# Performance work log

Hardware: AMD Instinct MI355X
Metric: run time of the kernel (lower is better)

## Reference

```python
import jax, jax.numpy as jnp
import numpy as np

EPS = 1e-5
GROUPS = 32


def group_norm(x, gamma, beta):
    b, c, h, w = x.shape
    xg = x.reshape(b, GROUPS, c // GROUPS, h, w)
    mu = xg.mean(axis=(2, 3, 4), keepdims=True)
    var = xg.var(axis=(2, 3, 4), keepdims=True)
    xn = ((xg - mu) * jax.lax.rsqrt(var + EPS)).reshape(b, c, h, w)
    return xn * gamma[None, :, None, None] + beta[None, :, None, None]


def setup_inputs() -> dict:
    key = jax.random.key(0)
    ks = jax.random.split(key, 4)
    b, c, h, w = 4, 512, 64, 64
    x = jax.random.normal(ks[0], (b, c, h, w), dtype=jnp.float32)
    gn_w = jnp.ones((c,), jnp.float32)
    gn_b = jnp.zeros((c,), jnp.float32)
    qkv_w = jax.random.normal(ks[1], (3 * c, c), dtype=jnp.float32) * (c ** -0.5)
    qkv_b = jnp.zeros((3 * c,), jnp.float32)
    out_w = jax.random.normal(ks[2], (c, c), dtype=jnp.float32) * (c ** -0.5)
    out_b = jnp.zeros((c,), jnp.float32)
    return {"x": x, "gn_w": gn_w, "gn_b": gn_b, "qkv_w": qkv_w,
            "qkv_b": qkv_b, "out_w": out_w, "out_b": out_b}


def reference(x, gn_w, gn_b, qkv_w, qkv_b, out_w, out_b):
    b, c, hh, ww = x.shape
    n = hh * ww
    h = group_norm(x, gn_w, gn_b)
    # 1x1 conv == per-pixel matmul over channels
    qkv = jnp.einsum('bchw,oc->bohw', h, qkv_w) + qkv_b[None, :, None, None]
    q, k, v = jnp.split(qkv, 3, axis=1)
    q = q.transpose(0, 2, 3, 1).reshape(b, n, c)   # (b, n, c)
    k = k.reshape(b, c, n)                          # (b, c, n)
    v = v.transpose(0, 2, 3, 1).reshape(b, n, c)   # (b, n, c)
    attn = jax.nn.softmax(jnp.einsum('bnc,bcm->bnm', q, k) * (c ** -0.5), axis=-1)
    out = jnp.einsum('bnm,bmc->bnc', attn, v)
    out = out.reshape(b, hh, ww, c).transpose(0, 3, 1, 2)
    out = jnp.einsum('bchw,oc->bohw', out, out_w) + out_b[None, :, None, None]
    return out + x
```

## Files before the change

kernel.cpp:

```cpp
#include <hip/hip_runtime.h>
#include <cmath>

#define NB 4
#define NC 512
#define NN 4096
#define ATTN_SCALE 0.04419417382415922f

typedef __bf16 bf16x8 __attribute__((ext_vector_type(8)));
typedef float floatx4 __attribute__((ext_vector_type(4)));

__device__ __forceinline__ unsigned short f2bf(float f) {
    union { float f; unsigned int u; } v; v.f = f;
    return (unsigned short)((v.u + 0x7fffu + ((v.u >> 16) & 1u)) >> 16);
}
__device__ __forceinline__ unsigned short f2bf_trunc(float f) {
    union { float f; unsigned int u; } v; v.f = f;
    return (unsigned short)(v.u >> 16);
}
__device__ __forceinline__ float bf2f(unsigned short u) {
    union { unsigned int u; float f; } v; v.u = ((unsigned int)u) << 16;
    return v.f;
}

__device__ __forceinline__ void gload_lds16(const unsigned short* gp, unsigned short* lp) {
    __builtin_amdgcn_global_load_lds(
        (const __attribute__((address_space(1))) void*)gp,
        (__attribute__((address_space(3))) void*)lp, 16, 0, 0);
}

__global__ __launch_bounds__(256) void gn_partial_kernel(
    const float* __restrict__ x, float* __restrict__ part)
{
    int blk = blockIdx.x;
    int bg = blk >> 3, sub = blk & 7;
    const float4* xv = (const float4*)(x + (size_t)bg * 16 * NN + (size_t)sub * 8192);
    float s1 = 0.f, s2 = 0.f;
#pragma unroll
    for (int i = 0; i < 8; ++i) {
        float4 v = xv[threadIdx.x + i * 256];
        s1 += v.x + v.y + v.z + v.w;
        s2 += v.x * v.x + v.y * v.y + v.z * v.z + v.w * v.w;
    }
#pragma unroll
    for (int off = 32; off; off >>= 1) {
        s1 += __shfl_xor(s1, off, 64);
        s2 += __shfl_xor(s2, off, 64);
    }
    __shared__ float r1[4], r2[4];
    int lane = threadIdx.x & 63, w = threadIdx.x >> 6;
    if (lane == 0) { r1[w] = s1; r2[w] = s2; }
    __syncthreads();
    if (threadIdx.x == 0) {
        part[blk * 2]     = r1[0] + r1[1] + r1[2] + r1[3];
        part[blk * 2 + 1] = r2[0] + r2[1] + r2[2] + r2[3];
    }
}

__global__ __launch_bounds__(128) void gn_final_kernel(
    const float* __restrict__ part, const float* __restrict__ gw,
    const float* __restrict__ gb, float* __restrict__ ss)
{
    int tg = threadIdx.x;
    int b = tg >> 5, g = tg & 31;
    float s1 = 0.f, s2 = 0.f;
#pragma unroll
    for (int s = 0; s < 8; ++s) {
        s1 += part[(tg * 8 + s) * 2];
        s2 += part[(tg * 8 + s) * 2 + 1];
    }
    float mean = s1 * (1.0f / 65536.0f);
    float var  = s2 * (1.0f / 65536.0f) - mean * mean;
    float rstd = rsqrtf(var + 1e-5f);
#pragma unroll
    for (int i = 0; i < 16; ++i) {
        int c = g * 16 + i;
        float sc = rstd * gw[c];
        ss[b * NC + c] = sc;
        ss[2048 + b * NC + c] = gb[c] - mean * sc;
    }
}

__global__ __launch_bounds__(256) void wconv_kernel(
    const float* __restrict__ qkv_w, const float* __restrict__ out_w,
    unsigned short* __restrict__ wq, unsigned short* __restrict__ wo)
{
    int i = blockIdx.x * 256 + threadIdx.x;
    const int NQ = 1536 * 512;
    if (i < NQ) wq[i] = f2bf(qkv_w[i]);
    else        wo[i - NQ] = f2bf(out_w[i - NQ]);
}

__global__ __launch_bounds__(256) void htnorm_kernel(
    const float* __restrict__ x, const float* __restrict__ ss,
    unsigned short* __restrict__ ht)
{
    int b = blockIdx.z;
    int c0 = blockIdx.y * 32, n0 = blockIdx.x * 32;
    __shared__ float T[32][33];
    int tx = threadIdx.x & 31, ty = threadIdx.x >> 5;
    const float* xb = x + ((size_t)b * NC + c0) * NN;
    const float* sc = ss + b * NC + c0;
    const float* sh = ss + 2048 + b * NC + c0;
#pragma unroll
    for (int i = 0; i < 4; ++i) {
        int c = ty + i * 8;
        T[c][tx] = xb[(size_t)c * NN + n0 + tx] * sc[c] + sh[c];
    }
    __syncthreads();
    unsigned short* hb = ht + ((size_t)b * NN + n0) * NC + c0;
#pragma unroll
    for (int i = 0; i < 4; ++i) {
        int n = ty + i * 8;
        hb[(size_t)n * NC + tx] = f2bf(T[tx][n]);
    }
}

template<int MODE, int BM, int BN>
__global__ __launch_bounds__(256, 3) void mfma_gemm(
    const unsigned short* __restrict__ Abase,
    const unsigned short* __restrict__ Bbase,
    const float* __restrict__ e0, const float* __restrict__ e1,
    float* __restrict__ outf,
    unsigned short* __restrict__ ob0, unsigned short* __restrict__ ob1)
{
    constexpr int K = 512;
    constexpr int FI = BM / 32;
    constexpr int FJ = BN / 32;
    const int z = blockIdx.z;
    const size_t bnc = (size_t)NN * NC;
    const size_t bss = (size_t)NN * NN;

    const unsigned short* A;
    const unsigned short* B;
    if constexpr (MODE == 0)      { A = Abase + (size_t)z * bnc; B = Bbase; }
    else if constexpr (MODE == 1) { A = Abase; B = Bbase + (size_t)z * bnc; }
    else if constexpr (MODE == 2) { A = Abase + (size_t)z * bnc; B = Bbase + (size_t)z * bnc; }
    else                          { A = Abase; B = Bbase + (size_t)z * bnc; }

    const int m0 = blockIdx.y * BM;
    const int n0 = blockIdx.x * BN;

    __shared__ __attribute__((aligned(16))) unsigned short As[BM * 32];
    __shared__ __attribute__((aligned(16))) unsigned short Bs[BN * 32];

    const int t = threadIdx.x;
    const int lane = t & 63;
    const int w = t >> 6;
    const int wr = w >> 1, wc = w & 1;

    const int sr = w * 16 + (lane >> 2);
    const int sc8 = (lane & 3) * 8;
    const int lds_elem = w * 512;

    floatx4 acc[FI][FJ] = {};

    for (int k0 = 0; k0 < K; k0 += 32) {
#pragma unroll
        for (int s = 0; s < BM / 64; ++s)
            gload_lds16(A + (size_t)(m0 + s * 64 + sr) * K + k0 + sc8,
                        As + s * 2048 + lds_elem);
#pragma unroll
        for (int s = 0; s < BN / 64; ++s)
            gload_lds16(B + (size_t)(n0 + s * 64 + sr) * K + k0 + sc8,
                        Bs + s * 2048 + lds_elem);
        __syncthreads();

        bf16x8 af[FI], bfr[FJ];
        const unsigned short* Ab = As + ((wr * (BM / 2) + (lane & 15)) * 32) + (lane >> 4) * 8;
        const unsigned short* Bb = Bs + ((wc * (BN / 2) + (lane & 15)) * 32) + (lane >> 4) * 8;
#pragma unroll
        for (int i = 0; i < FI; ++i) af[i]  = *(const bf16x8*)(Ab + i * 16 * 32);
#pragma unroll
        for (int j = 0; j < FJ; ++j) bfr[j] = *(const bf16x8*)(Bb + j * 16 * 32);
#pragma unroll
        for (int i = 0; i < FI; ++i)
#pragma unroll
            for (int j = 0; j < FJ; ++j)
                acc[i][j] = __builtin_amdgcn_mfma_f32_16x16x32_bf16(
                    af[i], bfr[j], acc[i][j], 0, 0, 0);
        __syncthreads();
    }

    const int fr = lane >> 4;
    const int fc = lane & 15;

    if constexpr (MODE == 2) {
        float rs[FI][4];
#pragma unroll
        for (int i = 0; i < FI; ++i)
#pragma unroll
            for (int r = 0; r < 4; ++r) rs[i][r] = 0.f;
#pragma unroll
        for (int i = 0; i < FI; ++i) {
#pragma unroll
            for (int j = 0; j < FJ; ++j) {
                int n = n0 + wc * (BN / 2) + j * 16 + fc;
                int mbase = m0 + wr * (BM / 2) + i * 16 + fr * 4;
#pragma unroll
                for (int r = 0; r < 4; ++r) {
                    float e = __expf(acc[i][j][r]);
                    ob0[(size_t)z * bss + (size_t)(mbase + r) * NN + n] = f2bf_trunc(e);
                    rs[i][r] += e;
                }
            }
        }
#pragma unroll
        for (int i = 0; i < FI; ++i) {
#pragma unroll
            for (int r = 0; r < 4; ++r) {
                float v = rs[i][r];
                v += __shfl_xor(v, 1, 16);
                v += __shfl_xor(v, 2, 16);
                v += __shfl_xor(v, 4, 16);
                v += __shfl_xor(v, 8, 16);
                if (fc == 0) {
                    int m = m0 + wr * (BM / 2) + i * 16 + fr * 4 + r;
                    atomicAdd(&outf[z * NN + m], v);
                }
            }
        }
        return;
    }

#pragma unroll
    for (int i = 0; i < FI; ++i) {
#pragma unroll
        for (int j = 0; j < FJ; ++j) {
            int n = n0 + wc * (BN / 2) + j * 16 + fc;
            int mbase = m0 + wr * (BM / 2) + i * 16 + fr * 4;
#pragma unroll
            for (int r = 0; r < 4; ++r) {
                int m = mbase + r;
                float val = acc[i][j][r];
                if constexpr (MODE == 0) {
                    val += e0[n];
                    if (n < 512) ob0[((size_t)z * NN + m) * NC + n] = f2bf(val * ATTN_SCALE);
                    else         ob1[((size_t)z * NN + m) * NC + (n - 512)] = f2bf(val);
                } else if constexpr (MODE == 1) {
                    val += e0[1024 + m];
                    ob0[((size_t)z * NC + m) * NN + n] = f2bf(val);
                } else {
                    size_t idx = ((size_t)z * NC + m) * NN + n;
                    outf[idx] = val + e0[m] + e1[idx];
                }
            }
        }
    }
}

__global__ __launch_bounds__(256, 3) void pv_gemm(
    const unsigned short* __restrict__ Abase,
    const unsigned short* __restrict__ Bbase,
    const float* __restrict__ L,
    unsigned short* __restrict__ Ob)
{
    const int z = blockIdx.z;
    const size_t bss = (size_t)NN * NN, bnc = (size_t)NN * NC;
    const unsigned short* A = Abase + (size_t)z * bss;
    const unsigned short* B = Bbase + (size_t)z * bnc;
    const int m0 = blockIdx.y * 64;
    const int n0 = blockIdx.x * 256;

    __shared__ __attribute__((aligned(16))) unsigned short As[64 * 32];
    __shared__ __attribute__((aligned(16))) unsigned short Bs[256 * 32];

    const int t = threadIdx.x;
    const int lane = t & 63;
    const int w = t >> 6;
    const int wr = w >> 1, wc = w & 1;
    const int sr = w * 16 + (lane >> 2);
    const int sc8 = (lane & 3) * 8;
    const int lds_elem = w * 512;

    floatx4 acc[2][8] = {};

    for (int k0 = 0; k0 < NN; k0 += 32) {
        gload_lds16(A + (size_t)(m0 + sr) * NN + k0 + sc8, As + lds_elem);
#pragma unroll
        for (int s = 0; s < 4; ++s)
            gload_lds16(B + (size_t)(n0 + s * 64 + sr) * NN + k0 + sc8,
                        Bs + s * 2048 + lds_elem);
        __syncthreads();

        bf16x8 af[2], bfr[8];
        const unsigned short* Ab = As + ((wr * 32 + (lane & 15)) * 32) + (lane >> 4) * 8;
        const unsigned short* Bb = Bs + ((wc * 128 + (lane & 15)) * 32) + (lane >> 4) * 8;
#pragma unroll
        for (int i = 0; i < 2; ++i) af[i]  = *(const bf16x8*)(Ab + i * 16 * 32);
#pragma unroll
        for (int j = 0; j < 8; ++j) bfr[j] = *(const bf16x8*)(Bb + j * 16 * 32);
#pragma unroll
        for (int i = 0; i < 2; ++i)
#pragma unroll
            for (int j = 0; j < 8; ++j)
                acc[i][j] = __builtin_amdgcn_mfma_f32_16x16x32_bf16(
                    af[i], bfr[j], acc[i][j], 0, 0, 0);
        __syncthreads();
    }

    const int fr = lane >> 4;
    const int fc = lane & 15;
#pragma unroll
    for (int i = 0; i < 2; ++i) {
#pragma unroll
        for (int r = 0; r < 4; ++r) {
            int m = m0 + wr * 32 + i * 16 + fr * 4 + r;
            float linv = 1.0f / L[z * NN + m];
#pragma unroll
            for (int j = 0; j < 8; ++j) {
                int n = n0 + wc * 128 + j * 16 + fc;
                Ob[(size_t)z * bnc + (size_t)m * NC + n] = f2bf(acc[i][j][r] * linv);
            }
        }
    }
}

extern "C" void kernel_launch(void* const* d_in, const int* in_sizes, int n_in,
                              void* d_out, int out_size, void* d_ws, size_t ws_size,
                              hipStream_t stream)
{
    const float* x     = (const float*)d_in[0];
    const float* gn_w  = (const float*)d_in[1];
    const float* gn_b  = (const float*)d_in[2];
    const float* qkv_w = (const float*)d_in[3];
    const float* qkv_b = (const float*)d_in[4];
    const float* out_w = (const float*)d_in[5];
    const float* out_b = (const float*)d_in[6];
    float* out = (float*)d_out;

    const size_t bnc = (size_t)NN * NC;
    char* w = (char*)d_ws;
    float* ss   = (float*)w;                 w += 16384;
    float* part = (float*)w;                 w += 8192;
    float* Lsum = (float*)w;                 w += (size_t)NB * NN * 4;
    unsigned short* wq = (unsigned short*)w; w += (size_t)1536 * 512 * 2;
    unsigned short* wo = (unsigned short*)w; w += (size_t)512 * 512 * 2;
    unsigned short* qt = (unsigned short*)w; w += NB * bnc * 2;
    unsigned short* kt = (unsigned short*)w; w += NB * bnc * 2;
    unsigned short* vt = (unsigned short*)w; w += NB * bnc * 2;
    unsigned short* SP = (unsigned short*)w; w += (size_t)NB * NN * NN * 2;
    unsigned short* ht = SP;
    unsigned short* Ob = qt;

    hipMemsetAsync(Lsum, 0, (size_t)NB * NN * sizeof(float), stream);

    gn_partial_kernel<<<1024, 256, 0, stream>>>(x, part);
    gn_final_kernel<<<1, 128, 0, stream>>>(part, gn_w, gn_b, ss);
    wconv_kernel<<<(1536 * 512 + 512 * 512) / 256, 256, 0, stream>>>(qkv_w, out_w, wq, wo);
    htnorm_kernel<<<dim3(NN / 32, NC / 32, NB), 256, 0, stream>>>(x, ss, ht);

    mfma_gemm<0, 128, 128><<<dim3(1024 / 128, NN / 128, NB), 256, 0, stream>>>(
        ht, wq, qkv_b, nullptr, nullptr, qt, kt);
    mfma_gemm<1, 128, 128><<<dim3(NN / 128, 512 / 128, NB), 256, 0, stream>>>(
        wq + (size_t)1024 * 512, ht, qkv_b, nullptr, nullptr, vt, nullptr);

    mfma_gemm<2, 128, 128><<<dim3(NN / 128, NN / 128, NB), 256, 0, stream>>>(
        qt, kt, nullptr, nullptr, Lsum, SP, nullptr);
    pv_gemm<<<dim3(512 / 256, NN / 64, NB), 256, 0, stream>>>(SP, vt, Lsum, Ob);

    mfma_gemm<4, 128, 128><<<dim3(NN / 128, 512 / 128, NB), 256, 0, stream>>>(
        wo, Ob, out_b, x, out, nullptr, nullptr);
}
```

Measured before the change: 412.0 us.

## Retile PV GEMM with XOR-swizzled LDS, deeper K step, and XCD-aware block mapping

The P·V GEMM moves from a 64x256 tile with K=32 to a 64x128 tile with K=64, using an XOR swizzle on the LDS row layout to avoid bank conflicts on fragment reads. The grid is flattened to 1024 blocks and remapped so the four column tiles sharing the same P rows land on the same XCD, improving L2 reuse of the large SP matrix. Occupancy target rises to 4 blocks/SM with fewer accumulators. Narrower tiles mean SP rows are read twice as often overall, relying on cache locality to offset that.

```diff
diff --git a/kernel.cpp b/kernel.cpp
--- a/kernel.cpp
+++ b/kernel.cpp
@@ -248,53 +248,76 @@
     }
 }
 
-__global__ __launch_bounds__(256, 3) void pv_gemm(
+__global__ __launch_bounds__(256, 4) void pv_gemm(
     const unsigned short* __restrict__ Abase,
     const unsigned short* __restrict__ Bbase,
     const float* __restrict__ L,
     unsigned short* __restrict__ Ob)
 {
-    const int z = blockIdx.z;
+    const int id = blockIdx.x;
+    const int xcd = id & 7;
+    const int j0 = id >> 3;
+    const int ct = j0 & 3;
+    const int pairl = j0 >> 2;
+    const int p = pairl * 8 + xcd;
+    const int ptile = p & 63, z = p >> 6;
+
     const size_t bss = (size_t)NN * NN, bnc = (size_t)NN * NC;
     const unsigned short* A = Abase + (size_t)z * bss;
     const unsigned short* B = Bbase + (size_t)z * bnc;
-    const int m0 = blockIdx.y * 64;
-    const int n0 = blockIdx.x * 256;
-
-    __shared__ __attribute__((aligned(16))) unsigned short As[64 * 32];
-    __shared__ __attribute__((aligned(16))) unsigned short Bs[256 * 32];
+    const int m0 = ptile * 64;
+    const int n0 = ct * 128;
+
+    __shared__ __attribute__((aligned(16))) unsigned short As[64 * 64];
+    __shared__ __attribute__((aligned(16))) unsigned short Bs[128 * 64];
 
     const int t = threadIdx.x;
     const int lane = t & 63;
     const int w = t >> 6;
     const int wr = w >> 1, wc = w & 1;
-    const int sr = w * 16 + (lane >> 2);
-    const int sc8 = (lane & 3) * 8;
+
+    const int sr = w * 8 + (lane >> 3);
+    const int scs = ((lane & 7) ^ (lane >> 3)) * 8;
     const int lds_elem = w * 512;
 
-    floatx4 acc[2][8] = {};
-
-    for (int k0 = 0; k0 < NN; k0 += 32) {
-        gload_lds16(A + (size_t)(m0 + sr) * NN + k0 + sc8, As + lds_elem);
+    floatx4 acc[2][4] = {};
+
+    for (int k0 = 0; k0 < NN; k0 += 64) {
+#pragma unroll
+        for (int s = 0; s < 2; ++s)
+            gload_lds16(A + (size_t)(m0 + s * 32 + sr) * NN + k0 + scs,
+                        As + s * 2048 + lds_elem);
 #pragma unroll
         for (int s = 0; s < 4; ++s)
-            gload_lds16(B + (size_t)(n0 + s * 64 + sr) * NN + k0 + sc8,
+            gload_lds16(B + (size_t)(n0 + s * 32 + sr) * NN + k0 + scs,
                         Bs + s * 2048 + lds_elem);
         __syncthreads();
 
-        bf16x8 af[2], bfr[8];
-        const unsigned short* Ab = As + ((wr * 32 + (lane & 15)) * 32) + (lane >> 4) * 8;
-        const unsigned short* Bb = Bs + ((wc * 128 + (lane & 15)) * 32) + (lane >> 4) * 8;
-#pragma unroll
-        for (int i = 0; i < 2; ++i) af[i]  = *(const bf16x8*)(Ab + i * 16 * 32);
-#pragma unroll
-        for (int j = 0; j < 8; ++j) bfr[j] = *(const bf16x8*)(Bb + j * 16 * 32);
-#pragma unroll
-        for (int i = 0; i < 2; ++i)
-#pragma unroll
-            for (int j = 0; j < 8; ++j)
-                acc[i][j] = __builtin_amdgcn_mfma_f32_16x16x32_bf16(
-                    af[i], bfr[j], acc[i][j], 0, 0, 0);
+        bf16x8 af[2][2], bfr[4][2];
+#pragma unroll
+        for (int i = 0; i < 2; ++i) {
+            const int ra = wr * 32 + i * 16 + (lane & 15);
+#pragma unroll
+            for (int kk = 0; kk < 2; ++kk)
+                af[i][kk] = *(const bf16x8*)(As + ra * 64 +
+                    (((kk * 4 + (lane >> 4)) ^ (ra & 7)) * 8));
+        }
+#pragma unroll
+        for (int jj = 0; jj < 4; ++jj) {
+            const int rb = wc * 64 + jj * 16 + (lane & 15);
+#pragma unroll
+            for (int kk = 0; kk < 2; ++kk)
+                bfr[jj][kk] = *(const bf16x8*)(Bs + rb * 64 +
+                    (((kk * 4 + (lane >> 4)) ^ (rb & 7)) * 8));
+        }
+#pragma unroll
+        for (int kk = 0; kk < 2; ++kk)
+#pragma unroll
+            for (int i = 0; i < 2; ++i)
+#pragma unroll
+                for (int jj = 0; jj < 4; ++jj)
+                    acc[i][jj] = __builtin_amdgcn_mfma_f32_16x16x32_bf16(
+                        af[i][kk], bfr[jj][kk], acc[i][jj], 0, 0, 0);
         __syncthreads();
     }
 
@@ -307,9 +330,9 @@
             int m = m0 + wr * 32 + i * 16 + fr * 4 + r;
             float linv = 1.0f / L[z * NN + m];
 #pragma unroll
-            for (int j = 0; j < 8; ++j) {
-                int n = n0 + wc * 128 + j * 16 + fc;
-                Ob[(size_t)z * bnc + (size_t)m * NC + n] = f2bf(acc[i][j][r] * linv);
+            for (int jj = 0; jj < 4; ++jj) {
+                int n = n0 + wc * 64 + jj * 16 + fc;
+                Ob[(size_t)z * bnc + (size_t)m * NC + n] = f2bf(acc[i][jj][r] * linv);
             }
         }
     }
@@ -356,7 +379,7 @@
 
     mfma_gemm<2, 128, 128><<<dim3(NN / 128, NN / 128, NB), 256, 0, stream>>>(
         qt, kt, nullptr, nullptr, Lsum, SP, nullptr);
-    pv_gemm<<<dim3(512 / 256, NN / 64, NB), 256, 0, stream>>>(SP, vt, Lsum, Ob);
+    pv_gemm<<<dim3(1024), 256, 0, stream>>>(SP, vt, Lsum, Ob);
 
     mfma_gemm<4, 128, 128><<<dim3(NN / 128, 512 / 128, NB), 256, 0, stream>>>(
         wo, Ob, out_b, x, out, nullptr, nullptr);
```

Result: faster. 378.2 us (-8.2%).

## Multi-buffer GEMM K-loop with swizzled LDS and XCD-aware block remapping

Applied to the files above, without the earlier changes.

Turns the shared GEMM template into a 3–4 stage pipeline. Asynchronous global-to-LDS loads for future K tiles are issued while MFMA work runs on the current tile, with explicit vmcnt waits and raw barriers replacing the double __syncthreads. It also XOR-swizzles the LDS column layout to cut bank conflicts, and remaps block ids so neighbouring tiles land on the same XCD for L2 reuse. The separate PV kernel is folded into the template as MODE 5 with smaller tiles. The cost is more LDS per block, which can lower occupancy, and hand-counted waitcnt values that must match the number of loads per stage.

```diff
diff --git a/kernel.cpp b/kernel.cpp
--- a/kernel.cpp
+++ b/kernel.cpp
@@ -17,15 +17,18 @@
     union { float f; unsigned int u; } v; v.f = f;
     return (unsigned short)(v.u >> 16);
 }
-__device__ __forceinline__ float bf2f(unsigned short u) {
-    union { unsigned int u; float f; } v; v.u = ((unsigned int)u) << 16;
-    return v.f;
-}
 
 __device__ __forceinline__ void gload_lds16(const unsigned short* gp, unsigned short* lp) {
     __builtin_amdgcn_global_load_lds(
         (const __attribute__((address_space(1))) void*)gp,
         (__attribute__((address_space(3))) void*)lp, 16, 0, 0);
+}
+
+template<int N> __device__ __forceinline__ void wait_vmcnt() {
+    if constexpr (N == 0) asm volatile("s_waitcnt vmcnt(0)" ::: "memory");
+    else if constexpr (N == 3) asm volatile("s_waitcnt vmcnt(3)" ::: "memory");
+    else if constexpr (N == 4) asm volatile("s_waitcnt vmcnt(4)" ::: "memory");
+    else if constexpr (N == 6) asm volatile("s_waitcnt vmcnt(6)" ::: "memory");
 }
 
 __global__ __launch_bounds__(256) void gn_partial_kernel(
@@ -115,33 +118,47 @@
     }
 }
 
-template<int MODE, int BM, int BN>
-__global__ __launch_bounds__(256, 3) void mfma_gemm(
+template<int MODE, int BM, int BN, int KD, int NBUF, int MINB>
+__global__ __launch_bounds__(256, MINB) void mfma_gemm(
     const unsigned short* __restrict__ Abase,
     const unsigned short* __restrict__ Bbase,
     const float* __restrict__ e0, const float* __restrict__ e1,
     float* __restrict__ outf,
     unsigned short* __restrict__ ob0, unsigned short* __restrict__ ob1)
 {
-    constexpr int K = 512;
+    constexpr int NT = KD / 32;
     constexpr int FI = BM / 32;
     constexpr int FJ = BN / 32;
-    const int z = blockIdx.z;
+    constexpr int LPS = BM / 64 + BN / 64;
+    constexpr int DEPTH = NBUF - 1;
     const size_t bnc = (size_t)NN * NC;
     const size_t bss = (size_t)NN * NN;
+
+    int z, m0, n0;
+    if constexpr (MODE == 2) {
+        const int id = blockIdx.x;
+        const int xcd = id & 7, j = id >> 3;
+        const int row = xcd * 16 + (j & 15);
+        z = row >> 5; m0 = (row & 31) * BM; n0 = (j >> 4) * BN;
+    } else if constexpr (MODE == 5) {
+        const int id = blockIdx.x;
+        const int xcd = id & 7, j0 = id >> 3;
+        const int p = (j0 >> 2) * 8 + xcd;
+        z = p >> 6; m0 = (p & 63) * BM; n0 = (j0 & 3) * BN;
+    } else {
+        z = blockIdx.z; m0 = blockIdx.y * BM; n0 = blockIdx.x * BN;
+    }
 
     const unsigned short* A;
     const unsigned short* B;
     if constexpr (MODE == 0)      { A = Abase + (size_t)z * bnc; B = Bbase; }
     else if constexpr (MODE == 1) { A = Abase; B = Bbase + (size_t)z * bnc; }
     else if constexpr (MODE == 2) { A = Abase + (size_t)z * bnc; B = Bbase + (size_t)z * bnc; }
+    else if constexpr (MODE == 5) { A = Abase + (size_t)z * bss; B = Bbase + (size_t)z * bnc; }
     else                          { A = Abase; B = Bbase + (size_t)z * bnc; }
 
-    const int m0 = blockIdx.y * BM;
-    const int n0 = blockIdx.x * BN;
-
-    __shared__ __attribute__((aligned(16))) unsigned short As[BM * 32];
-    __shared__ __attribute__((aligned(16))) unsigned short Bs[BN * 32];
+    __shared__ __attribute__((aligned(16))) unsigned short As[NBUF][BM * 32];
+    __shared__ __attribute__((aligned(16))) unsigned short Bs[NBUF][BN * 32];
 
     const int t = threadIdx.x;
     const int lane = t & 63;
@@ -149,36 +166,85 @@
     const int wr = w >> 1, wc = w & 1;
 
     const int sr = w * 16 + (lane >> 2);
-    const int sc8 = (lane & 3) * 8;
+    const int scs = ((lane & 3) ^ ((lane >> 3) & 3)) * 8;
     const int lds_elem = w * 512;
+    const int kslot = lane >> 4;
 
     floatx4 acc[FI][FJ] = {};
 
-    for (int k0 = 0; k0 < K; k0 += 32) {
+    auto stage = [&](int buf, int tile) {
+        const int k0 = tile * 32;
 #pragma unroll
         for (int s = 0; s < BM / 64; ++s)
-            gload_lds16(A + (size_t)(m0 + s * 64 + sr) * K + k0 + sc8,
-                        As + s * 2048 + lds_elem);
+            gload_lds16(A + (size_t)(m0 + s * 64 + sr) * KD + k0 + scs,
+                        &As[buf][s * 2048 + lds_elem]);
 #pragma unroll
         for (int s = 0; s < BN / 64; ++s)
-            gload_lds16(B + (size_t)(n0 + s * 64 + sr) * K + k0 + sc8,
-                        Bs + s * 2048 + lds_elem);
-        __syncthreads();
-
+            gload_lds16(B + (size_t)(n0 + s * 64 + sr) * KD + k0 + scs,
+                        &Bs[buf][s * 2048 + lds_elem]);
+    };
+
+    auto compute = [&](int buf) {
         bf16x8 af[FI], bfr[FJ];
-        const unsigned short* Ab = As + ((wr * (BM / 2) + (lane & 15)) * 32) + (lane >> 4) * 8;
-        const unsigned short* Bb = Bs + ((wc * (BN / 2) + (lane & 15)) * 32) + (lane >> 4) * 8;
-#pragma unroll
-        for (int i = 0; i < FI; ++i) af[i]  = *(const bf16x8*)(Ab + i * 16 * 32);
-#pragma unroll
-        for (int j = 0; j < FJ; ++j) bfr[j] = *(const bf16x8*)(Bb + j * 16 * 32);
+#pragma unroll
+        for (int i = 0; i < FI; ++i) {
+            const int ra = wr * (BM / 2) + i * 16 + (lane & 15);
+            af[i] = *(const bf16x8*)(&As[buf][ra * 32 + ((kslot ^ ((ra >> 1) & 3)) * 8)]);
+        }
+#pragma unroll
+        for (int j = 0; j < FJ; ++j) {
+            const int rb = wc * (BN / 2) + j * 16 + (lane & 15);
+            bfr[j] = *(const bf16x8*)(&Bs[buf][rb * 32 + ((kslot ^ ((rb >> 1) & 3)) * 8)]);
+        }
 #pragma unroll
         for (int i = 0; i < FI; ++i)
 #pragma unroll
             for (int j = 0; j < FJ; ++j)
                 acc[i][j] = __builtin_amdgcn_mfma_f32_16x16x32_bf16(
                     af[i], bfr[j], acc[i][j], 0, 0, 0);
-        __syncthreads();
+    };
+
+#pragma unroll
+    for (int d = 0; d < DEPTH; ++d) stage(d, d);
+    wait_vmcnt<(DEPTH - 1) * LPS>();
+    __builtin_amdgcn_s_barrier();
+
+    if constexpr (NT <= 16) {
+#pragma unroll
+        for (int kt = 0; kt < NT - DEPTH; ++kt) {
+            stage((kt + DEPTH) % NBUF, kt + DEPTH);
+            compute(kt % NBUF);
+            asm volatile("s_waitcnt lgkmcnt(0)" ::: "memory");
+            wait_vmcnt<(DEPTH - 1) * LPS>();
+            __builtin_amdgcn_s_barrier();
+        }
+    } else {
+#pragma unroll 4
+        for (int kt = 0; kt < NT - DEPTH; ++kt) {
+            stage((kt + DEPTH) & (NBUF - 1), kt + DEPTH);
+            compute(kt & (NBUF - 1));
+            asm volatile("s_waitcnt lgkmcnt(0)" ::: "memory");
+            wait_vmcnt<(DEPTH - 1) * LPS>();
+            __builtin_amdgcn_s_barrier();
+        }
+    }
+
+    if constexpr (DEPTH == 2) {
+        compute((NT - 2) % NBUF);
+        asm volatile("s_waitcnt lgkmcnt(0)" ::: "memory");
+        wait_vmcnt<0>();
+        __builtin_amdgcn_s_barrier();
+        compute((NT - 1) % NBUF);
+    } else {
+        compute((NT - 3) % NBUF);
+        asm volatile("s_waitcnt lgkmcnt(0)" ::: "memory");
+        wait_vmcnt<LPS>();
+        __builtin_amdgcn_s_barrier();
+        compute((NT - 2) % NBUF);
+        asm volatile("s_waitcnt lgkmcnt(0)" ::: "memory");
+        wait_vmcnt<0>();
+        __builtin_amdgcn_s_barrier();
+        compute((NT - 1) % NBUF);
     }
 
     const int fr = lane >> 4;
@@ -216,6 +282,23 @@
                 if (fc == 0) {
                     int m = m0 + wr * (BM / 2) + i * 16 + fr * 4 + r;
                     atomicAdd(&outf[z * NN + m], v);
+                }
+            }
+        }
+        return;
+    }
+
+    if constexpr (MODE == 5) {
+#pragma unroll
+        for (int i = 0; i < FI; ++i) {
+#pragma unroll
+            for (int r = 0; r < 4; ++r) {
+                int m = m0 + wr * (BM / 2) + i * 16 + fr * 4 + r;
+                float linv = 1.0f / e0[z * NN + m];
+#pragma unroll
+                for (int j = 0; j < FJ; ++j) {
+                    int n = n0 + wc * (BN / 2) + j * 16 + fc;
+                    ob0[(size_t)z * bnc + (size_t)m * NC + n] = f2bf(acc[i][j][r] * linv);
                 }
             }
         }
@@ -248,73 +331,6 @@
     }
 }
 
-__global__ __launch_bounds__(256, 3) void pv_gemm(
-    const unsigned short* __restrict__ Abase,
-    const unsigned short* __restrict__ Bbase,
-    const float* __restrict__ L,
-    unsigned short* __restrict__ Ob)
-{
-    const int z = blockIdx.z;
-    const size_t bss = (size_t)NN * NN, bnc = (size_t)NN * NC;
-    const unsigned short* A = Abase + (size_t)z * bss;
-    const unsigned short* B = Bbase + (size_t)z * bnc;
-    const int m0 = blockIdx.y * 64;
-    const int n0 = blockIdx.x * 256;
-
-    __shared__ __attribute__((aligned(16))) unsigned short As[64 * 32];
-    __shared__ __attribute__((aligned(16))) unsigned short Bs[256 * 32];
-
-    const int t = threadIdx.x;
-    const int lane = t & 63;
-    const int w = t >> 6;
-    const int wr = w >> 1, wc = w & 1;
-    const int sr = w * 16 + (lane >> 2);
-    const int sc8 = (lane & 3) * 8;
-    const int lds_elem = w * 512;
-
-    floatx4 acc[2][8] = {};
-
-    for (int k0 = 0; k0 < NN; k0 += 32) {
-        gload_lds16(A + (size_t)(m0 + sr) * NN + k0 + sc8, As + lds_elem);
-#pragma unroll
-        for (int s = 0; s < 4; ++s)
-            gload_lds16(B + (size_t)(n0 + s * 64 + sr) * NN + k0 + sc8,
-                        Bs + s * 2048 + lds_elem);
-        __syncthreads();
-
-        bf16x8 af[2], bfr[8];
-        const unsigned short* Ab = As + ((wr * 32 + (lane & 15)) * 32) + (lane >> 4) * 8;
-        const unsigned short* Bb = Bs + ((wc * 128 + (lane & 15)) * 32) + (lane >> 4) * 8;
-#pragma unroll
-        for (int i = 0; i < 2; ++i) af[i]  = *(const bf16x8*)(Ab + i * 16 * 32);
-#pragma unroll
-        for (int j = 0; j < 8; ++j) bfr[j] = *(const bf16x8*)(Bb + j * 16 * 32);
-#pragma unroll
-        for (int i = 0; i < 2; ++i)
-#pragma unroll
-            for (int j = 0; j < 8; ++j)
-                acc[i][j] = __builtin_amdgcn_mfma_f32_16x16x32_bf16(
-                    af[i], bfr[j], acc[i][j], 0, 0, 0);
-        __syncthreads();
-    }
-
-    const int fr = lane >> 4;
-    const int fc = lane & 15;
-#pragma unroll
-    for (int i = 0; i < 2; ++i) {
-#pragma unroll
-        for (int r = 0; r < 4; ++r) {
-            int m = m0 + wr * 32 + i * 16 + fr * 4 + r;
-            float linv = 1.0f / L[z * NN + m];
-#pragma unroll
-            for (int j = 0; j < 8; ++j) {
-                int n = n0 + wc * 128 + j * 16 + fc;
-                Ob[(size_t)z * bnc + (size_t)m * NC + n] = f2bf(acc[i][j][r] * linv);
-            }
-        }
-    }
-}
-
 extern "C" void kernel_launch(void* const* d_in, const int* in_sizes, int n_in,
                               void* d_out, int out_size, void* d_ws, size_t ws_size,
                               hipStream_t stream)
@@ -349,15 +365,16 @@
     wconv_kernel<<<(1536 * 512 + 512 * 512) / 256, 256, 0, stream>>>(qkv_w, out_w, wq, wo);
     htnorm_kernel<<<dim3(NN / 32, NC / 32, NB), 256, 0, stream>>>(x, ss, ht);
 
-    mfma_gemm<0, 128, 128><<<dim3(1024 / 128, NN / 128, NB), 256, 0, stream>>>(
+    mfma_gemm<0, 128, 128, 512, 3, 3><<<dim3(1024 / 128, NN / 128, NB), 256, 0, stream>>>(
         ht, wq, qkv_b, nullptr, nullptr, qt, kt);
-    mfma_gemm<1, 128, 128><<<dim3(NN / 128, 512 / 128, NB), 256, 0, stream>>>(
+    mfma_gemm<1, 64, 128, 512, 3, 4><<<dim3(NN / 128, 512 / 64, NB), 256, 0, stream>>>(
         wq + (size_t)1024 * 512, ht, qkv_b, nullptr, nullptr, vt, nullptr);
 
-    mfma_gemm<2, 128, 128><<<dim3(NN / 128, NN / 128, NB), 256, 0, stream>>>(
+    mfma_gemm<2, 128, 128, 512, 3, 3><<<dim3(4096), 256, 0, stream>>>(
         qt, kt, nullptr, nullptr, Lsum, SP, nullptr);
-    pv_gemm<<<dim3(512 / 256, NN / 64, NB), 256, 0, stream>>>(SP, vt, Lsum, Ob);
-
-    mfma_gemm<4, 128, 128><<<dim3(NN / 128, 512 / 128, NB), 256, 0, stream>>>(
+    mfma_gemm<5, 64, 128, 4096, 4, 3><<<dim3(1024), 256, 0, stream>>>(
+        SP, vt, Lsum, nullptr, nullptr, Ob, nullptr);
+
+    mfma_gemm<4, 64, 128, 512, 3, 4><<<dim3(NN / 128, 512 / 64, NB), 256, 0, stream>>>(
         wo, Ob, out_b, x, out, nullptr, nullptr);
 }
```

Measured after the change: 418.1 us. No clear change (+1.5%).
